# Optimization experiments

Measured on AMD Instinct MI355X. Metric: run time of the kernel, lower is better.

The kernel has to match this reference:

```python
import jax, jax.numpy as jnp
import numpy as np

CHANNELS = 256
NUM_HEADS = 4
NUM_GROUPS = 8
EPS = 1e-5


def setup_inputs() -> dict:
    key = jax.random.key(0)
    ks = jax.random.split(key, 7)
    c = CHANNELS
    x = jax.random.normal(ks[0], (2, c, 16, 16, 16), dtype=jnp.float32)
    # GroupNorm affine params (torch init: weight=1, bias=0)
    norm_w = jnp.ones((c,), dtype=jnp.float32)
    norm_b = jnp.zeros((c,), dtype=jnp.float32)
    # 1x1x1 Conv3d weights stored as [out_ch, in_ch]
    fan = 1.0 / np.sqrt(c)
    qkv_w = jax.random.uniform(ks[1], (3 * c, c), minval=-fan, maxval=fan, dtype=jnp.float32)
    qkv_b = jax.random.uniform(ks[2], (3 * c,), minval=-fan, maxval=fan, dtype=jnp.float32)
    proj_w = jax.random.uniform(ks[3], (c, c), minval=-fan, maxval=fan, dtype=jnp.float32)
    proj_b = jax.random.uniform(ks[4], (c,), minval=-fan, maxval=fan, dtype=jnp.float32)
    return {"x": x, "norm_w": norm_w, "norm_b": norm_b,
            "qkv_w": qkv_w, "qkv_b": qkv_b, "proj_w": proj_w, "proj_b": proj_b}


def _group_norm(x, w, b):
    B, C, D, H, W = x.shape
    g = NUM_GROUPS
    xg = x.reshape(B, g, C // g, D, H, W)
    mean = xg.mean(axis=(2, 3, 4, 5), keepdims=True)
    var = xg.var(axis=(2, 3, 4, 5), keepdims=True)
    xg = (xg - mean) * jax.lax.rsqrt(var + EPS)
    x = xg.reshape(B, C, D, H, W)
    return x * w[None, :, None, None, None] + b[None, :, None, None, None]


def _conv1x1(x, w, b):
    # x: [B, Cin, D, H, W], w: [Cout, Cin]
    y = jnp.einsum('bcdhw,oc->bodhw', x, w)
    return y + b[None, :, None, None, None]


def reference(x, norm_w, norm_b, qkv_w, qkv_b, proj_w, proj_b):
    B, C, D, H, W = x.shape
    N = D * H * W
    hd = C // NUM_HEADS
    x_norm = _group_norm(x, norm_w, norm_b)
    qkv = _conv1x1(x_norm, qkv_w, qkv_b)  # [B, 3C, D, H, W]
    q, k, v = jnp.split(qkv, 3, axis=1)
    q = q.reshape(B, NUM_HEADS, hd, N)
    k = k.reshape(B, NUM_HEADS, hd, N)
    v = v.reshape(B, NUM_HEADS, hd, N)
    scale = hd ** -0.5
    # attn[b,h,n,m] = softmax_m(q[:, :, :, n] . k[:, :, :, m] * scale)
    scores = jnp.einsum('bhcn,bhcm->bhnm', q, k) * scale
    attn = jax.nn.softmax(scores, axis=-1)
    out = jnp.einsum('bhcm,bhnm->bhcn', v, attn)
    out = out.reshape(B, C, D, H, W)
    return _conv1x1(out, proj_w, proj_b) + x
```

## Files before the change

### kernel.cpp

```cpp
#include <hip/hip_runtime.h>
#include <hip/hip_bf16.h>

#define NSP 4096
#define CH 256
#define NB 2
#define NG 8
#define CPG 32
#define NHD 4
#define HDIM 64

typedef unsigned short u16;
typedef unsigned int u32;
typedef __attribute__((ext_vector_type(8))) short bf16x8;
typedef __attribute__((ext_vector_type(4))) float f32x4;

#define MFMA __builtin_amdgcn_mfma_f32_16x16x32_bf16
#define QSCALE 0.18033688f

__device__ __forceinline__ u16 f2bf(float f) {
    u32 i = __float_as_uint(f);
    u32 r = (i + 0x7FFFu + ((i >> 16) & 1u)) >> 16;
    return (u16)r;
}

__device__ __forceinline__ void dma16(const u16* g, u16* l) {
    __builtin_amdgcn_global_load_lds(
        (const __attribute__((address_space(1))) void*)g,
        (__attribute__((address_space(3))) void*)l, 16, 0, 0);
}

__global__ __launch_bounds__(256) void prep(const float* __restrict__ qw,
                                            const float* __restrict__ pw,
                                            u16* __restrict__ wqb,
                                            u16* __restrict__ wpb,
                                            const float* __restrict__ x,
                                            float* __restrict__ partial) {
    if (blockIdx.x < 256) {
        int i = (blockIdx.x * 256 + threadIdx.x) * 4;
        const float* src; u16* dst;
        if (i < 3 * CH * CH) { src = qw + i; dst = wqb + i; }
        else { src = pw + (i - 3 * CH * CH); dst = wpb + (i - 3 * CH * CH); }
        float4 v = *(const float4*)src;
        ushort4 o;
        o.x = f2bf(v.x); o.y = f2bf(v.y); o.z = f2bf(v.z); o.w = f2bf(v.w);
        *(ushort4*)dst = o;
        return;
    }
    const int id = blockIdx.x - 256;
    const int bg = id >> 4, chunk = id & 15;
    const float* p = x + (size_t)bg * (CPG * NSP) + chunk * 8192;
    float s = 0.f, ss = 0.f;
    for (int i = threadIdx.x; i < 2048; i += 256) {
        float4 u = ((const float4*)p)[i];
        s += u.x + u.y + u.z + u.w;
        ss += u.x * u.x + u.y * u.y + u.z * u.z + u.w * u.w;
    }
    for (int off = 32; off > 0; off >>= 1) {
        s += __shfl_down(s, off);
        ss += __shfl_down(ss, off);
    }
    __shared__ float red[4][2];
    const int wv = threadIdx.x >> 6;
    if ((threadIdx.x & 63) == 0) { red[wv][0] = s; red[wv][1] = ss; }
    __syncthreads();
    if (threadIdx.x == 0) {
        float ts = red[0][0] + red[1][0] + red[2][0] + red[3][0];
        float tq = red[0][1] + red[1][1] + red[2][1] + red[3][1];
        partial[(bg * 16 + chunk) * 2]     = ts;
        partial[(bg * 16 + chunk) * 2 + 1] = tq;
    }
}

__global__ __launch_bounds__(256) void gn_apply_t(const float* __restrict__ x,
                                                  const float* __restrict__ partial,
                                                  const float* __restrict__ w,
                                                  const float* __restrict__ b,
                                                  u16* __restrict__ xnT) {
    __shared__ u16 T[64][72];
    const int n0 = blockIdx.x * 64, c0 = blockIdx.y * 64, bb = blockIdx.z;
    const int t = threadIdx.x;
    const int rc = t & 63;
    const int g  = t >> 6;
    const int c  = c0 + rc;
    const int bg = bb * NG + c / CPG;
    float s = 0.f, q = 0.f;
#pragma unroll
    for (int j = 0; j < 16; ++j) {
        s += partial[(bg * 16 + j) * 2];
        q += partial[(bg * 16 + j) * 2 + 1];
    }
    const float cnt = (float)(CPG * NSP);
    float mean = s / cnt;
    float var  = q / cnt - mean * mean;
    float rstd = rsqrtf(var + 1e-5f);
    float wf = w[c] * rstd, bv = b[c] - mean * wf;
    const float* px = x + ((size_t)bb * CH + c) * NSP + n0 + g * 16;
#pragma unroll
    for (int i = 0; i < 4; ++i) {
        float4 v = *(const float4*)(px + i * 4);
        T[g * 16 + i * 4 + 0][rc] = f2bf(v.x * wf + bv);
        T[g * 16 + i * 4 + 1][rc] = f2bf(v.y * wf + bv);
        T[g * 16 + i * 4 + 2][rc] = f2bf(v.z * wf + bv);
        T[g * 16 + i * 4 + 3][rc] = f2bf(v.w * wf + bv);
    }
    __syncthreads();
    int n = t >> 2, ch = (t & 3) * 16;
    uint4 o0 = *(const uint4*)&T[n][ch];
    uint4 o1 = *(const uint4*)&T[n][ch + 8];
    u16* dst = xnT + ((size_t)bb * NSP + n0 + n) * CH + c0 + ch;
    *(uint4*)dst = o0;
    *(uint4*)(dst + 8) = o1;
}

__global__ __launch_bounds__(256) void gemm_qkv(const u16* __restrict__ Aw,
                                                const float* __restrict__ bias,
                                                const u16* __restrict__ xnT,
                                                u16* __restrict__ qT,
                                                u16* __restrict__ kT,
                                                u16* __restrict__ v) {
    const int n0 = blockIdx.x * 64, m0 = blockIdx.y * 64, bb = blockIdx.z;
    const int wave = threadIdx.x >> 6, lane = threadIdx.x & 63;
    const int lq = lane & 15, quad = lane >> 4;
    const int wm = (wave >> 1) * 32, wn = (wave & 1) * 32;
    f32x4 acc[2][2] = {};
    const u16* ap = Aw + (size_t)(m0 + wm + lq) * CH + quad * 8;
    const u16* bp = xnT + ((size_t)bb * NSP + n0 + wn + lq) * CH + quad * 8;
#pragma unroll
    for (int k0 = 0; k0 < CH; k0 += 32) {
        bf16x8 a0 = *(const bf16x8*)(ap + k0);
        bf16x8 a1 = *(const bf16x8*)(ap + 16 * CH + k0);
        bf16x8 b0 = *(const bf16x8*)(bp + k0);
        bf16x8 b1 = *(const bf16x8*)(bp + 16 * CH + k0);
        acc[0][0] = MFMA(a0, b0, acc[0][0], 0, 0, 0);
        acc[0][1] = MFMA(a0, b1, acc[0][1], 0, 0, 0);
        acc[1][0] = MFMA(a1, b0, acc[1][0], 0, 0, 0);
        acc[1][1] = MFMA(a1, b1, acc[1][1], 0, 0, 0);
    }
    const int sect = m0 >> 8;
    const int h = (m0 & 255) >> 6;
    const float osc = (sect == 0) ? QSCALE : 1.f;
#pragma unroll
    for (int im = 0; im < 2; ++im) {
        int ml = wm + im * 16 + quad * 4;
        float4 bs = *(const float4*)(bias + m0 + ml);
#pragma unroll
        for (int in = 0; in < 2; ++in) {
            int n = n0 + wn + in * 16 + lq;
            f32x4 a = acc[im][in];
            float v0 = (a[0] + bs.x) * osc, v1 = (a[1] + bs.y) * osc;
            float v2 = (a[2] + bs.z) * osc, v3 = (a[3] + bs.w) * osc;
            if (sect < 2) {
                int lc = ml >> 3, sub = ml & 7;
                int colp = ((lc ^ (n & 7)) << 3) | sub;
                u16* base = (sect ? kT : qT) +
                            (((size_t)bb * NHD + h) * NSP + n) * HDIM + colp;
                ushort4 o;
                o.x = f2bf(v0); o.y = f2bf(v1); o.z = f2bf(v2); o.w = f2bf(v3);
                *(ushort4*)base = o;
            } else {
                float vv[4] = {v0, v1, v2, v3};
#pragma unroll
                for (int r = 0; r < 4; ++r) {
                    int ch = (m0 - 512) + ml + r;
                    int pos = (n & ~63) + ((((n >> 3) & 7) ^ (ch & 7)) << 3) + (n & 7);
                    v[((size_t)bb * CH + ch) * NSP + pos] = f2bf(vv[r]);
                }
            }
        }
    }
}

__global__ __launch_bounds__(512, 2) void attn10(const u16* __restrict__ qT,
                                                 const u16* __restrict__ kT,
                                                 const u16* __restrict__ vN,
                                                 u16* __restrict__ aoT) {
    __shared__ u16 Ks[2][2][64][64];
    __shared__ u16 Vs[2][2][64][64];
    __shared__ __align__(16) char smem_ps[8 * 32 * 72 * 2];
    __shared__ float Ml[8][2][16];
    u16 (*Ps)[32][72] = reinterpret_cast<u16(*)[32][72]>(smem_ps);
    float (*Obuf)[32][68] = reinterpret_cast<float(*)[32][68]>(smem_ps);

    const int h = blockIdx.y, bb = blockIdx.z;
    const int t = threadIdx.x;
    const int wave = t >> 6, lane = t & 63;
    const int qg = wave & 3, kh = wave >> 2;
    const int lq = lane & 15, quad = lane >> 4;
    const int q_lo = blockIdx.x * 128 + qg * 32;

    const int pr = quad ^ (lq & 7);
    const u16* qrow0 = qT + (((size_t)bb * NHD + h) * NSP + q_lo + lq) * HDIM;
    bf16x8 qf[2][2];
    qf[0][0] = *(const bf16x8*)(qrow0 + pr * 8);
    qf[0][1] = *(const bf16x8*)(qrow0 + (pr ^ 4) * 8);
    qf[1][0] = *(const bf16x8*)(qrow0 + 16 * HDIM + pr * 8);
    qf[1][1] = *(const bf16x8*)(qrow0 + 16 * HDIM + (pr ^ 4) * 8);

    const u16* khead = kT + ((size_t)bb * NHD + h) * NSP * (size_t)HDIM;
    const u16* vhead = vN + ((size_t)bb * CH + h * HDIM) * NSP;

    const int sK   = (wave < 4);
    const int kh_s = (wave >> 1) & 1;
    const int rbase = (wave & 1) * 32;
    {
#pragma unroll
        for (int j = 0; j < 4; ++j) {
            int r8 = rbase + j * 8;
            if (sK) {
                dma16(khead + (size_t)(kh_s * 2048 + r8) * HDIM + lane * 8,
                      &Ks[kh_s][0][r8][0]);
            } else {
                dma16(vhead + (size_t)(r8 + (lane >> 3)) * NSP + kh_s * 2048 + (lane & 7) * 8,
                      &Vs[kh_s][0][r8][0]);
            }
        }
    }

    float l[2] = {0.f, 0.f};
    f32x4 O[2][4] = {};
    for (int kt = 0; kt < 32; ++kt) {
        const int cur = kt & 1;
        __syncthreads();
        if (kt < 31) {
            const int K1 = (kt + 1) * 64;
#pragma unroll
            for (int j = 0; j < 4; ++j) {
                int r8 = rbase + j * 8;
                if (sK) {
                    dma16(khead + (size_t)(kh_s * 2048 + K1 + r8) * HDIM + lane * 8,
                          &Ks[kh_s][cur ^ 1][r8][0]);
                } else {
                    dma16(vhead + (size_t)(r8 + (lane >> 3)) * NSP + kh_s * 2048 + K1 + (lane & 7) * 8,
                          &Vs[kh_s][cur ^ 1][r8][0]);
                }
            }
        }
        f32x4 st[2][4];
#pragma unroll
        for (int mt = 0; mt < 4; ++mt) {
            bf16x8 a0 = *(const bf16x8*)&Ks[kh][cur][mt * 16 + lq][pr * 8];
            bf16x8 a1 = *(const bf16x8*)&Ks[kh][cur][mt * 16 + lq][(pr ^ 4) * 8];
#pragma unroll
            for (int qt = 0; qt < 2; ++qt) {
                f32x4 acc = {0.f, 0.f, 0.f, 0.f};
                acc = MFMA(a0, qf[qt][0], acc, 0, 0, 0);
                acc = MFMA(a1, qf[qt][1], acc, 0, 0, 0);
                st[qt][mt] = acc;
            }
        }
#pragma unroll
        for (int qt = 0; qt < 2; ++qt) {
            float sum = 0.f;
#pragma unroll
            for (int mt = 0; mt < 4; ++mt) {
                float p0 = __builtin_amdgcn_exp2f(st[qt][mt][0]);
                float p1 = __builtin_amdgcn_exp2f(st[qt][mt][1]);
                float p2 = __builtin_amdgcn_exp2f(st[qt][mt][2]);
                float p3 = __builtin_amdgcn_exp2f(st[qt][mt][3]);
                sum += (p0 + p1) + (p2 + p3);
                u32 r0 = __float_as_uint(p0) + 0x8000u;
                u32 r1 = __float_as_uint(p1) + 0x8000u;
                u32 r2 = __float_as_uint(p2) + 0x8000u;
                u32 r3 = __float_as_uint(p3) + 0x8000u;
                uint2 pkk;
                pkk.x = __builtin_amdgcn_perm(r1, r0, 0x07060302);
                pkk.y = __builtin_amdgcn_perm(r3, r2, 0x07060302);
                *(uint2*)&Ps[wave][qt * 16 + lq][mt * 16 + quad * 4] = pkk;
            }
            l[qt] += sum;
        }
        bf16x8 pf[2][2];
        pf[0][0] = *(const bf16x8*)&Ps[wave][lq][quad * 8];
        pf[0][1] = *(const bf16x8*)&Ps[wave][lq][32 + quad * 8];
        pf[1][0] = *(const bf16x8*)&Ps[wave][16 + lq][quad * 8];
        pf[1][1] = *(const bf16x8*)&Ps[wave][16 + lq][32 + quad * 8];
#pragma unroll
        for (int mtc = 0; mtc < 4; ++mtc) {
            bf16x8 v0 = *(const bf16x8*)&Vs[kh][cur][mtc * 16 + lq][pr * 8];
            bf16x8 v1 = *(const bf16x8*)&Vs[kh][cur][mtc * 16 + lq][(pr ^ 4) * 8];
#pragma unroll
            for (int qt = 0; qt < 2; ++qt) {
                O[qt][mtc] = MFMA(v0, pf[qt][0], O[qt][mtc], 0, 0, 0);
                O[qt][mtc] = MFMA(v1, pf[qt][1], O[qt][mtc], 0, 0, 0);
            }
        }
    }
#pragma unroll
    for (int qt = 0; qt < 2; ++qt) {
        l[qt] += __shfl_xor(l[qt], 16);
        l[qt] += __shfl_xor(l[qt], 32);
    }
    if (lane < 16) { Ml[wave][0][lane] = l[0]; Ml[wave][1][lane] = l[1]; }
    __syncthreads();
    float gl[2];
    gl[0] = l[0] + Ml[wave ^ 4][0][lq];
    gl[1] = l[1] + Ml[wave ^ 4][1][lq];
    if (kh == 1) {
#pragma unroll
        for (int qt = 0; qt < 2; ++qt)
#pragma unroll
            for (int mtc = 0; mtc < 4; ++mtc)
                *(f32x4*)&Obuf[qg][qt * 16 + lq][mtc * 16 + quad * 4] = O[qt][mtc];
    }
    __syncthreads();
    if (kh == 0) {
#pragma unroll
        for (int qt = 0; qt < 2; ++qt) {
            float linv = 1.f / gl[qt];
            u16* op = aoT + ((size_t)bb * NSP + q_lo + qt * 16 + lq) * CH + h * HDIM;
#pragma unroll
            for (int mtc = 0; mtc < 4; ++mtc) {
                f32x4 sres = O[qt][mtc] +
                             *(const f32x4*)&Obuf[qg][qt * 16 + lq][mtc * 16 + quad * 4];
                ushort4 o;
                o.x = f2bf(sres[0] * linv);
                o.y = f2bf(sres[1] * linv);
                o.z = f2bf(sres[2] * linv);
                o.w = f2bf(sres[3] * linv);
                *(ushort4*)(op + mtc * 16 + quad * 4) = o;
            }
        }
    }
}

__global__ __launch_bounds__(256) void gemm_proj(const u16* __restrict__ Aw,
                                                 const float* __restrict__ bias,
                                                 const u16* __restrict__ aoT,
                                                 const float* __restrict__ xres,
                                                 float* __restrict__ out) {
    const int n0 = blockIdx.x * 64, m0 = blockIdx.y * 64, bb = blockIdx.z;
    const int wave = threadIdx.x >> 6, lane = threadIdx.x & 63;
    const int lq = lane & 15, quad = lane >> 4;
    const int wm = (wave >> 1) * 32, wn = (wave & 1) * 32;
    f32x4 acc[2][2] = {};
    const u16* ap = Aw + (size_t)(m0 + wm + lq) * CH + quad * 8;
    const u16* bp = aoT + ((size_t)bb * NSP + n0 + wn + lq) * CH + quad * 8;
#pragma unroll
    for (int k0 = 0; k0 < CH; k0 += 32) {
        bf16x8 a0 = *(const bf16x8*)(ap + k0);
        bf16x8 a1 = *(const bf16x8*)(ap + 16 * CH + k0);
        bf16x8 b0 = *(const bf16x8*)(bp + k0);
        bf16x8 b1 = *(const bf16x8*)(bp + 16 * CH + k0);
        acc[0][0] = MFMA(a0, b0, acc[0][0], 0, 0, 0);
        acc[0][1] = MFMA(a0, b1, acc[0][1], 0, 0, 0);
        acc[1][0] = MFMA(a1, b0, acc[1][0], 0, 0, 0);
        acc[1][1] = MFMA(a1, b1, acc[1][1], 0, 0, 0);
    }
#pragma unroll
    for (int im = 0; im < 2; ++im) {
        int ml = wm + im * 16 + quad * 4;
        float4 bs = *(const float4*)(bias + m0 + ml);
        float bsv[4] = {bs.x, bs.y, bs.z, bs.w};
#pragma unroll
        for (int in = 0; in < 2; ++in) {
            int n = n0 + wn + in * 16 + lq;
            f32x4 a = acc[im][in];
#pragma unroll
            for (int r = 0; r < 4; ++r) {
                size_t idx = ((size_t)bb * CH + m0 + ml + r) * NSP + n;
                out[idx] = a[r] + bsv[r] + xres[idx];
            }
        }
    }
}

extern "C" void kernel_launch(void* const* d_in, const int* in_sizes, int n_in,
                              void* d_out, int out_size, void* d_ws, size_t ws_size,
                              hipStream_t stream) {
    const float* x      = (const float*)d_in[0];
    const float* norm_w = (const float*)d_in[1];
    const float* norm_b = (const float*)d_in[2];
    const float* qkv_w  = (const float*)d_in[3];
    const float* qkv_b  = (const float*)d_in[4];
    const float* proj_w = (const float*)d_in[5];
    const float* proj_b = (const float*)d_in[6];
    float* out = (float*)d_out;

    char* w = (char*)d_ws;
    float* partial = (float*)w;
    u16* wqb = (u16*)(w + 4096);
    u16* wpb = (u16*)(w + 4096 + 393216);
    u16* xnT = (u16*)(w + 528384);
    u16* qT  = (u16*)(w + 528384 + 4194304);
    u16* kT  = (u16*)(w + 528384 + 2 * 4194304);
    u16* v   = (u16*)(w + 528384 + 3 * 4194304);
    u16* aoT = xnT;

    prep<<<dim3(512), 256, 0, stream>>>(qkv_w, proj_w, wqb, wpb, x, partial);
    gn_apply_t<<<dim3(NSP / 64, CH / 64, NB), 256, 0, stream>>>(
        x, partial, norm_w, norm_b, xnT);
    gemm_qkv<<<dim3(NSP / 64, (3 * CH) / 64, NB), 256, 0, stream>>>(
        wqb, qkv_b, xnT, qT, kT, v);
    attn10<<<dim3(NSP / 128, NHD, NB), 512, 0, stream>>>(qT, kT, v, aoT);
    gemm_proj<<<dim3(NSP / 64, CH / 64, NB), 256, 0, stream>>>(
        wpb, proj_b, aoT, x, out);
}
```

Before: 163.5 us.

## Stage QKV/proj GEMM operands in LDS via async DMA with XOR-swizzled layouts

The QKV and output-projection GEMMs now copy the full 64x256 A and B tiles into shared memory with global_load_lds DMA, then feed the MFMAs from LDS instead of issuing strided global loads. To keep those LDS reads free of bank conflicts, the producers (weight conversion, normalized-activation transpose and attention output) now write their bf16 data in an XOR-swizzled column order that matches the consumers. This cuts redundant global traffic and latency in the GEMM inner loop. In exchange it uses 64 KB of LDS per block, which may limit occupancy, and it couples several kernels to the same swizzle convention.

Result: faster. 143.6 us (median of 2 runs) (-12.2%).

```diff
diff --git a/kernel.cpp b/kernel.cpp
--- a/kernel.cpp
+++ b/kernel.cpp
@@ -37,13 +37,15 @@
                                             float* __restrict__ partial) {
     if (blockIdx.x < 256) {
         int i = (blockIdx.x * 256 + threadIdx.x) * 4;
-        const float* src; u16* dst;
-        if (i < 3 * CH * CH) { src = qw + i; dst = wqb + i; }
-        else { src = pw + (i - 3 * CH * CH); dst = wpb + (i - 3 * CH * CH); }
+        const float* src; u16* dstbase; int j;
+        if (i < 3 * CH * CH) { src = qw + i; dstbase = wqb; j = i; }
+        else { j = i - 3 * CH * CH; src = pw + j; dstbase = wpb; }
+        int m = j >> 8, c = j & 255;
+        int dc = ((((c >> 3) ^ (m & 7)) << 3)) | (c & 7);
         float4 v = *(const float4*)src;
         ushort4 o;
         o.x = f2bf(v.x); o.y = f2bf(v.y); o.z = f2bf(v.z); o.w = f2bf(v.w);
-        *(ushort4*)dst = o;
+        *(ushort4*)(dstbase + (m << 8) + dc) = o;
         return;
     }
     const int id = blockIdx.x - 256;
@@ -107,34 +109,48 @@
     int n = t >> 2, ch = (t & 3) * 16;
     uint4 o0 = *(const uint4*)&T[n][ch];
     uint4 o1 = *(const uint4*)&T[n][ch + 8];
-    u16* dst = xnT + ((size_t)bb * NSP + n0 + n) * CH + c0 + ch;
-    *(uint4*)dst = o0;
-    *(uint4*)(dst + 8) = o1;
-}
-
-__global__ __launch_bounds__(256) void gemm_qkv(const u16* __restrict__ Aw,
-                                                const float* __restrict__ bias,
-                                                const u16* __restrict__ xnT,
-                                                u16* __restrict__ qT,
-                                                u16* __restrict__ kT,
-                                                u16* __restrict__ v) {
+    const int sw = n & 7;
+    const int chunk0 = (c0 + ch) >> 3;
+    u16* rowp = xnT + ((size_t)bb * NSP + n0 + n) * CH;
+    *(uint4*)(rowp + ((chunk0 ^ sw) << 3))       = o0;
+    *(uint4*)(rowp + (((chunk0 + 1) ^ sw) << 3)) = o1;
+}
+
+__global__ __launch_bounds__(256, 2) void gemm_qkv(const u16* __restrict__ Aw,
+                                                   const float* __restrict__ bias,
+                                                   const u16* __restrict__ xnT,
+                                                   u16* __restrict__ qT,
+                                                   u16* __restrict__ kT,
+                                                   u16* __restrict__ v) {
+    __shared__ u16 As[64][256];
+    __shared__ u16 Bs[64][256];
     const int n0 = blockIdx.x * 64, m0 = blockIdx.y * 64, bb = blockIdx.z;
     const int wave = threadIdx.x >> 6, lane = threadIdx.x & 63;
     const int lq = lane & 15, quad = lane >> 4;
+#pragma unroll
+    for (int j = 0; j < 8; ++j) {
+        int r2 = (wave * 8 + j) * 2;
+        dma16(Aw + (size_t)(m0 + r2) * CH + lane * 8, &As[r2][0]);
+        dma16(xnT + ((size_t)bb * NSP + n0 + r2) * CH + lane * 8, &Bs[r2][0]);
+    }
+    __syncthreads();
     const int wm = (wave >> 1) * 32, wn = (wave & 1) * 32;
+    const int sw = lq & 7;
     f32x4 acc[2][2] = {};
-    const u16* ap = Aw + (size_t)(m0 + wm + lq) * CH + quad * 8;
-    const u16* bp = xnT + ((size_t)bb * NSP + n0 + wn + lq) * CH + quad * 8;
-#pragma unroll
-    for (int k0 = 0; k0 < CH; k0 += 32) {
-        bf16x8 a0 = *(const bf16x8*)(ap + k0);
-        bf16x8 a1 = *(const bf16x8*)(ap + 16 * CH + k0);
-        bf16x8 b0 = *(const bf16x8*)(bp + k0);
-        bf16x8 b1 = *(const bf16x8*)(bp + 16 * CH + k0);
-        acc[0][0] = MFMA(a0, b0, acc[0][0], 0, 0, 0);
-        acc[0][1] = MFMA(a0, b1, acc[0][1], 0, 0, 0);
-        acc[1][0] = MFMA(a1, b0, acc[1][0], 0, 0, 0);
-        acc[1][1] = MFMA(a1, b1, acc[1][1], 0, 0, 0);
+#pragma unroll
+    for (int kk = 0; kk < 8; ++kk) {
+        bf16x8 a[2], b[2];
+#pragma unroll
+        for (int mt = 0; mt < 2; ++mt)
+            a[mt] = *(const bf16x8*)&As[wm + mt * 16 + lq][(((kk * 4 + quad) ^ sw)) << 3];
+#pragma unroll
+        for (int nt = 0; nt < 2; ++nt)
+            b[nt] = *(const bf16x8*)&Bs[wn + nt * 16 + lq][(((kk * 4 + quad) ^ sw)) << 3];
+#pragma unroll
+        for (int mt = 0; mt < 2; ++mt)
+#pragma unroll
+            for (int nt = 0; nt < 2; ++nt)
+                acc[mt][nt] = MFMA(a[mt], b[nt], acc[mt][nt], 0, 0, 0);
     }
     const int sect = m0 >> 8;
     const int h = (m0 & 255) >> 6;
@@ -304,10 +320,11 @@
     }
     __syncthreads();
     if (kh == 0) {
+        const int sw = lq & 7;
 #pragma unroll
         for (int qt = 0; qt < 2; ++qt) {
             float linv = 1.f / gl[qt];
-            u16* op = aoT + ((size_t)bb * NSP + q_lo + qt * 16 + lq) * CH + h * HDIM;
+            u16* rowp = aoT + ((size_t)bb * NSP + q_lo + qt * 16 + lq) * CH;
 #pragma unroll
             for (int mtc = 0; mtc < 4; ++mtc) {
                 f32x4 sres = O[qt][mtc] +
@@ -317,34 +334,48 @@
                 o.y = f2bf(sres[1] * linv);
                 o.z = f2bf(sres[2] * linv);
                 o.w = f2bf(sres[3] * linv);
-                *(ushort4*)(op + mtc * 16 + quad * 4) = o;
-            }
-        }
-    }
-}
-
-__global__ __launch_bounds__(256) void gemm_proj(const u16* __restrict__ Aw,
-                                                 const float* __restrict__ bias,
-                                                 const u16* __restrict__ aoT,
-                                                 const float* __restrict__ xres,
-                                                 float* __restrict__ out) {
+                int chunk = (h << 3) | (mtc << 1) | (quad >> 1);
+                int col = ((chunk ^ sw) << 3) | ((quad & 1) << 2);
+                *(ushort4*)(rowp + col) = o;
+            }
+        }
+    }
+}
+
+__global__ __launch_bounds__(256, 2) void gemm_proj(const u16* __restrict__ Aw,
+                                                    const float* __restrict__ bias,
+                                                    const u16* __restrict__ aoT,
+                                                    const float* __restrict__ xres,
+                                                    float* __restrict__ out) {
+    __shared__ u16 As[64][256];
+    __shared__ u16 Bs[64][256];
     const int n0 = blockIdx.x * 64, m0 = blockIdx.y * 64, bb = blockIdx.z;
     const int wave = threadIdx.x >> 6, lane = threadIdx.x & 63;
     const int lq = lane & 15, quad = lane >> 4;
+#pragma unroll
+    for (int j = 0; j < 8; ++j) {
+        int r2 = (wave * 8 + j) * 2;
+        dma16(Aw + (size_t)(m0 + r2) * CH + lane * 8, &As[r2][0]);
+        dma16(aoT + ((size_t)bb * NSP + n0 + r2) * CH + lane * 8, &Bs[r2][0]);
+    }
+    __syncthreads();
     const int wm = (wave >> 1) * 32, wn = (wave & 1) * 32;
+    const int sw = lq & 7;
     f32x4 acc[2][2] = {};
-    const u16* ap = Aw + (size_t)(m0 + wm + lq) * CH + quad * 8;
-    const u16* bp = aoT + ((size_t)bb * NSP + n0 + wn + lq) * CH + quad * 8;
-#pragma unroll
-    for (int k0 = 0; k0 < CH; k0 += 32) {
-        bf16x8 a0 = *(const bf16x8*)(ap + k0);
-        bf16x8 a1 = *(const bf16x8*)(ap + 16 * CH + k0);
-        bf16x8 b0 = *(const bf16x8*)(bp + k0);
-        bf16x8 b1 = *(const bf16x8*)(bp + 16 * CH + k0);
-        acc[0][0] = MFMA(a0, b0, acc[0][0], 0, 0, 0);
-        acc[0][1] = MFMA(a0, b1, acc[0][1], 0, 0, 0);
-        acc[1][0] = MFMA(a1, b0, acc[1][0], 0, 0, 0);
-        acc[1][1] = MFMA(a1, b1, acc[1][1], 0, 0, 0);
+#pragma unroll
+    for (int kk = 0; kk < 8; ++kk) {
+        bf16x8 a[2], b[2];
+#pragma unroll
+        for (int mt = 0; mt < 2; ++mt)
+            a[mt] = *(const bf16x8*)&As[wm + mt * 16 + lq][(((kk * 4 + quad) ^ sw)) << 3];
+#pragma unroll
+        for (int nt = 0; nt < 2; ++nt)
+            b[nt] = *(const bf16x8*)&Bs[wn + nt * 16 + lq][(((kk * 4 + quad) ^ sw)) << 3];
+#pragma unroll
+        for (int mt = 0; mt < 2; ++mt)
+#pragma unroll
+            for (int nt = 0; nt < 2; ++nt)
+                acc[mt][nt] = MFMA(a[mt], b[nt], acc[mt][nt], 0, 0, 0);
     }
 #pragma unroll
     for (int im = 0; im < 2; ++im) {
```
